# Optimization experiments

Hardware: AMD Instinct MI355X
Metric: run time of the kernel (lower is better)

## Reference

```python
import jax, jax.numpy as jnp
import numpy as np
import math

N_EMBD = 1024
N_HEAD = 16
HEAD_SIZE = N_EMBD // N_HEAD
LAYER_IDX = 2
LAMBDA_INIT = 0.8 - 0.6 * math.exp(-0.3 * (LAYER_IDX - 1))
LN_EPS = 1e-5
B, T = 4, 1024


def setup_inputs() -> dict:
    key = jax.random.key(0)
    ks = jax.random.split(key, 11)
    s = 0.02  # weight init scale
    return {
        "x": jax.random.normal(ks[0], (B, T, N_EMBD), dtype=jnp.float32),
        "Wq1": jax.random.normal(ks[1], (N_EMBD, N_EMBD), dtype=jnp.float32) * s,
        "Wq2": jax.random.normal(ks[2], (N_EMBD, N_EMBD), dtype=jnp.float32) * s,
        "Wk1": jax.random.normal(ks[3], (N_EMBD, N_EMBD), dtype=jnp.float32) * s,
        "Wk2": jax.random.normal(ks[4], (N_EMBD, N_EMBD), dtype=jnp.float32) * s,
        "Wv": jax.random.normal(ks[5], (N_EMBD, 2 * N_EMBD), dtype=jnp.float32) * s,
        "Wc": jax.random.normal(ks[6], (2 * N_EMBD, N_EMBD), dtype=jnp.float32) * s,
        "lq1": jax.random.normal(ks[7], (N_HEAD, HEAD_SIZE), dtype=jnp.float32) * 0.1,
        "lk1": jax.random.normal(ks[8], (N_HEAD, HEAD_SIZE), dtype=jnp.float32) * 0.1,
        "lq2": jax.random.normal(ks[9], (N_HEAD, HEAD_SIZE), dtype=jnp.float32) * 0.1,
        "lk2": jax.random.normal(ks[10], (N_HEAD, HEAD_SIZE), dtype=jnp.float32) * 0.1,
    }


def reference(x, Wq1, Wq2, Wk1, Wk2, Wv, Wc, lq1, lk1, lq2, lk2):
    Bx, Tx, C = x.shape
    H, hs = N_HEAD, HEAD_SIZE
    scale = 1.0 / math.sqrt(hs)

    # projections -> (B, T, H, d)
    q1 = (x @ Wq1).reshape(Bx, Tx, H, hs)
    q2 = (x @ Wq2).reshape(Bx, Tx, H, hs)
    k1 = (x @ Wk1).reshape(Bx, Tx, H, hs)
    k2 = (x @ Wk2).reshape(Bx, Tx, H, hs)
    v = (x @ Wv).reshape(Bx, Tx, H, 2 * hs)

    # dual score streams (B, H, T, T)
    att1 = jnp.einsum("bqhd,bkhd->bhqk", q1, k1) * scale
    att2 = jnp.einsum("bqhd,bkhd->bhqk", q2, k2) * scale

    causal = jnp.tril(jnp.ones((Tx, Tx), dtype=bool))  # (T, T)
    neg_inf = jnp.float32(-jnp.inf)
    att1 = jnp.where(causal, att1, neg_inf)
    att2 = jnp.where(causal, att2, neg_inf)
    a1 = jax.nn.softmax(att1, axis=-1)
    a2 = jax.nn.softmax(att2, axis=-1)

    # per-head differential lambda
    lam1 = jnp.exp(jnp.sum(lq1 * lk1, axis=-1))  # (H,)
    lam2 = jnp.exp(jnp.sum(lq2 * lk2, axis=-1))  # (H,)
    lam_full = lam1 - lam2 + LAMBDA_INIT  # (H,)

    att = a1 - lam_full[None, :, None, None] * a2  # dropout = identity (eval)

    # PV matmul -> (B, T, H, 2*hs)
    y = jnp.einsum("bhqk,bkhd->bqhd", att, v)

    # subLN over last dim (no affine)
    mu = jnp.mean(y, axis=-1, keepdims=True)
    var = jnp.mean(jnp.square(y - mu), axis=-1, keepdims=True)
    y = (y - mu) / jnp.sqrt(var + LN_EPS)
    y = y * (1.0 - LAMBDA_INIT)

    y = y.reshape(Bx, Tx, 2 * C)
    return y @ Wc  # resid dropout = identity (eval)
```

## Files before the change

kernel.cpp:

```cpp
#include <hip/hip_runtime.h>


#define T_SEQ 1024
#define NH 16
#define DV 128
#define NPROJ 6144
#define KSTR 72

typedef __bf16 bf16_t;
typedef __bf16 bf16x8 __attribute__((ext_vector_type(8)));
typedef __bf16 bf16x4 __attribute__((ext_vector_type(4)));
typedef float f32x4 __attribute__((ext_vector_type(4)));

#define LAMBDA_INIT 0.35550906759096928f
#define ONE_MINUS_LI 0.6444909324090307f
#define LOG2E 1.4426950408889634f

#define GLDS(g, l)                                                            \
  __builtin_amdgcn_global_load_lds(                                           \
      (const __attribute__((address_space(1))) void*)(g),                     \
      (__attribute__((address_space(3))) void*)(l), 16, 0, 0)

template <int C>
__device__ __forceinline__ float dppf(float x) {
  return __builtin_bit_cast(
      float, __builtin_amdgcn_update_dpp(0, __builtin_bit_cast(int, x), C,
                                         0xF, 0xF, true));
}
__device__ __forceinline__ float row16_max(float x) {
  x = fmaxf(x, dppf<0xB1>(x));
  x = fmaxf(x, dppf<0x4E>(x));
  x = fmaxf(x, dppf<0x124>(x));
  x = fmaxf(x, dppf<0x128>(x));
  return x;
}
__device__ __forceinline__ float row16_sum(float x) {
  x += dppf<0xB1>(x);
  x += dppf<0x4E>(x);
  x += dppf<0x124>(x);
  x += dppf<0x128>(x);
  return x;
}

static const size_t OFF_WCAT = 0;
static const size_t OFF_XB = OFF_WCAT + (size_t)6144 * 1024 * 2;
static const size_t OFF_WCT = OFF_XB + (size_t)4096 * 1024 * 2;
static const size_t OFF_PROJ = OFF_WCT + (size_t)2048 * 1024 * 2;
static const size_t OFF_VT = OFF_PROJ + (size_t)4096 * 6144 * 2;
static const size_t OFF_YLN = OFF_VT + (size_t)64 * 128 * 1024 * 2;
static const size_t OFF_LAM = OFF_YLN + (size_t)4096 * 2048 * 2;

__global__ void __launch_bounds__(256) cast_x(const float* __restrict__ x,
                                              bf16_t* __restrict__ o) {
  const int i = (blockIdx.x * 256 + threadIdx.x) * 4;
  float4 v = *(const float4*)(x + i);
  bf16x4 r = {(bf16_t)v.x, (bf16_t)v.y, (bf16_t)v.z, (bf16_t)v.w};
  *(bf16x4*)(o + i) = r;
}

__device__ __forceinline__ void tcast_body(const float* __restrict__ W,
                                           bf16_t* __restrict__ Wt, int K,
                                           int N, int row0) {
  __shared__ float tile[32][33];
  const int k0 = blockIdx.x * 32, n0 = blockIdx.y * 32;
  const int tx = threadIdx.x & 31, ty = threadIdx.x >> 5;
#pragma unroll
  for (int i = 0; i < 32; i += 8)
    tile[ty + i][tx] = W[(long)(k0 + ty + i) * N + n0 + tx];
  __syncthreads();
#pragma unroll
  for (int i = 0; i < 32; i += 8)
    Wt[(long)(row0 + n0 + ty + i) * K + k0 + tx] = (bf16_t)tile[tx][ty + i];
}

__global__ void __launch_bounds__(256) tcast_w(const float* __restrict__ W,
                                               bf16_t* __restrict__ Wt, int K,
                                               int N, int row0) {
  tcast_body(W, Wt, K, N, row0);
}

__global__ void __launch_bounds__(256) tcast_w4(const float* __restrict__ W0,
                                                const float* __restrict__ W1,
                                                const float* __restrict__ W2,
                                                const float* __restrict__ W3,
                                                bf16_t* __restrict__ Wt) {
  const float* Ws[4] = {W0, W1, W2, W3};
  tcast_body(Ws[blockIdx.z], Wt, 1024, 1024, blockIdx.z * 1024);
}

__global__ void lam_kernel(const float* __restrict__ lq1,
                           const float* __restrict__ lk1,
                           const float* __restrict__ lq2,
                           const float* __restrict__ lk2,
                           float* __restrict__ lam) {
  const int h = threadIdx.x;
  if (h < NH) {
    float d1 = 0.f, d2 = 0.f;
    for (int i = 0; i < 64; ++i) {
      d1 += lq1[h * 64 + i] * lk1[h * 64 + i];
      d2 += lq2[h * 64 + i] * lk2[h * 64 + i];
    }
    lam[h] = expf(d1) - expf(d2) + LAMBDA_INIT;
  }
}

#define BM 128
#define BN 128
#define BK 32

template <typename OutT>
__global__ void __launch_bounds__(256) gemm_bt(const bf16_t* __restrict__ A,
                                               const bf16_t* __restrict__ Bt,
                                               OutT* __restrict__ C, int M,
                                               int N, int K) {
  __shared__ __align__(16) bf16_t As[BM * BK];
  __shared__ __align__(16) bf16_t Bs[BN * BK];
  const int tid = threadIdx.x;
  const int w = tid >> 6;
  const int lane = tid & 63;
  const int quad = lane >> 4, l16 = lane & 15;
  const int m0 = blockIdx.y * BM, n0 = blockIdx.x * BN;
  const int wm = (w >> 1) * 64, wn = (w & 1) * 64;
  const int srow = tid >> 2;
  const int scol = (tid & 3) * 8;

  const bf16_t* Ag0 = A + (long)(m0 + srow) * K + scol;
  const bf16_t* Ag1 = Ag0 + (long)64 * K;
  const bf16_t* Bg0 = Bt + (long)(n0 + srow) * K + scol;
  const bf16_t* Bg1 = Bg0 + (long)64 * K;
  bf16_t* lA0 = As + tid * 8;
  bf16_t* lA1 = As + 2048 + tid * 8;
  bf16_t* lB0 = Bs + tid * 8;
  bf16_t* lB1 = Bs + 2048 + tid * 8;

  f32x4 acc[4][4] = {};

  for (int k0 = 0; k0 < K; k0 += BK) {
    GLDS(Ag0 + k0, lA0);
    GLDS(Ag1 + k0, lA1);
    GLDS(Bg0 + k0, lB0);
    GLDS(Bg1 + k0, lB1);
    __syncthreads();
    bf16x8 af[4], bfr[4];
#pragma unroll
    for (int t = 0; t < 4; ++t) {
      af[t] = *(const bf16x8*)(As + (wm + t * 16 + l16) * BK + quad * 8);
      bfr[t] = *(const bf16x8*)(Bs + (wn + t * 16 + l16) * BK + quad * 8);
    }
#pragma unroll
    for (int mt = 0; mt < 4; ++mt)
#pragma unroll
      for (int nt = 0; nt < 4; ++nt)
        acc[mt][nt] = __builtin_amdgcn_mfma_f32_16x16x32_bf16(
            af[mt], bfr[nt], acc[mt][nt], 0, 0, 0);
    __syncthreads();
  }

#pragma unroll
  for (int mt = 0; mt < 4; ++mt)
#pragma unroll
    for (int nt = 0; nt < 4; ++nt) {
      const int col = n0 + wn + nt * 16 + l16;
#pragma unroll
      for (int i = 0; i < 4; ++i) {
        const int row = m0 + wm + mt * 16 + quad * 4 + i;
        C[(long)row * N + col] = (OutT)acc[mt][nt][i];
      }
    }
}

__global__ void __launch_bounds__(256) transpose_v(const bf16_t* __restrict__ proj,
                                                   bf16_t* __restrict__ vt) {
  __shared__ bf16_t tile[32][34];
  const int bh = blockIdx.z;
  const int b = bh >> 4, h = bh & 15;
  const int t0 = blockIdx.x * 32, d0 = blockIdx.y * 32;
  const int tx = threadIdx.x & 31, ty = threadIdx.x >> 5;
  const bf16_t* src = proj + (long)(b * T_SEQ) * NPROJ + 4096 + h * 128;
#pragma unroll
  for (int i = 0; i < 32; i += 8)
    tile[ty + i][tx] = src[(long)(t0 + ty + i) * NPROJ + d0 + tx];
  __syncthreads();
  bf16_t* dst = vt + ((long)(b * NH + h) * DV) * T_SEQ;
#pragma unroll
  for (int i = 0; i < 32; i += 8)
    dst[(long)(d0 + ty + i) * T_SEQ + t0 + tx] = tile[tx][ty + i];
}

__global__ void __launch_bounds__(256) attn_kernel(const bf16_t* __restrict__ proj,
                                                   const bf16_t* __restrict__ vt,
                                                   const float* __restrict__ lamp,
                                                   bf16_t* __restrict__ yln) {
  const int p = blockIdx.x;
  const int h = blockIdx.y;
  const int b = blockIdx.z;
  const int tid = threadIdx.x;
  const int w = tid >> 6, lane = tid & 63;
  const int quad = lane >> 4, l16 = lane & 15;
  const long bT = (long)b * T_SEQ;

  __shared__ __align__(16) bf16_t Ks1[32 * KSTR];
  __shared__ __align__(16) bf16_t Ks2[32 * KSTR];
  __shared__ __align__(16) bf16_t Vs[DV * 32];
  __shared__ __align__(16) bf16_t pbuf[4][2][16 * 40];

  const bf16_t* gK1 =
      proj + (bT + (tid >> 3)) * (long)NPROJ + h * 64 + 2048 + (tid & 7) * 8;
  const bf16_t* gK2 = gK1 + 1024;
  const bf16_t* vbase = vt + ((long)(b * NH + h) * DV) * T_SEQ;
  const bf16_t* gV0 = vbase + (long)(tid >> 2) * T_SEQ + (tid & 3) * 8;
  const bf16_t* gV1 = gV0 + (long)64 * T_SEQ;
  const int kw = (tid >> 3) * KSTR + (tid & 7) * 8;

  bf16_t* pb1 = &pbuf[w][0][0];
  bf16_t* pb2 = &pbuf[w][1][0];
  const float sc = 0.125f * LOG2E;
  const float lam = lamp[h];
  const int prd = l16 * 40 + ((quad ^ (l16 >> 2)) << 3);

  for (int phase = 0; phase < 2; ++phase) {
    const int qblk = phase == 0 ? (15 - p) : p;
    const int q0 = qblk * 64 + w * 16;

    const bf16_t* qrow = proj + (bT + q0 + l16) * (long)NPROJ + h * 64;
    bf16x8 aq1[2], aq2[2];
    aq1[0] = *(const bf16x8*)(qrow + quad * 8);
    aq1[1] = *(const bf16x8*)(qrow + 32 + quad * 8);
    aq2[0] = *(const bf16x8*)(qrow + 1024 + quad * 8);
    aq2[1] = *(const bf16x8*)(qrow + 1024 + 32 + quad * 8);

    f32x4 O1[8] = {}, O2[8] = {};
    float m1[4], l1[4], m2[4], l2[4];
#pragma unroll
    for (int i = 0; i < 4; ++i) {
      m1[i] = -3.0e38f;
      m2[i] = -3.0e38f;
      l1[i] = 0.f;
      l2[i] = 0.f;
    }

    const int kend_blk = qblk * 64 + 64;
    const int kend_w = q0 + 16;

    bf16x8 rK1 = *(const bf16x8*)(gK1);
    bf16x8 rK2 = *(const bf16x8*)(gK2);
    bf16x8 rV0 = *(const bf16x8*)(gV0);
    bf16x8 rV1 = *(const bf16x8*)(gV1);

    for (int kt = 0; kt < kend_blk; kt += 32) {
      *(bf16x8*)(Ks1 + kw) = rK1;
      *(bf16x8*)(Ks2 + kw) = rK2;
      *(bf16x8*)(Vs + tid * 8) = rV0;
      *(bf16x8*)(Vs + 2048 + tid * 8) = rV1;
      __syncthreads();

      if (kt + 32 < kend_blk) {
        const long ko = (long)(kt + 32) * NPROJ;
        rK1 = *(const bf16x8*)(gK1 + ko);
        rK2 = *(const bf16x8*)(gK2 + ko);
        rV0 = *(const bf16x8*)(gV0 + kt + 32);
        rV1 = *(const bf16x8*)(gV1 + kt + 32);
      }

      if (kt < kend_w) {
        f32x4 s1[2], s2[2];
#pragma unroll
        for (int c = 0; c < 2; ++c) {
          const bf16_t* kr1 = Ks1 + (c * 16 + l16) * KSTR;
          const bf16_t* kr2 = Ks2 + (c * 16 + l16) * KSTR;
          bf16x8 b10 = *(const bf16x8*)(kr1 + quad * 8);
          bf16x8 b11 = *(const bf16x8*)(kr1 + 32 + quad * 8);
          f32x4 z = {};
          z = __builtin_amdgcn_mfma_f32_16x16x32_bf16(aq1[0], b10, z, 0, 0, 0);
          z = __builtin_amdgcn_mfma_f32_16x16x32_bf16(aq1[1], b11, z, 0, 0, 0);
          s1[c] = z;
          bf16x8 b20 = *(const bf16x8*)(kr2 + quad * 8);
          bf16x8 b21 = *(const bf16x8*)(kr2 + 32 + quad * 8);
          f32x4 z2 = {};
          z2 = __builtin_amdgcn_mfma_f32_16x16x32_bf16(aq2[0], b20, z2, 0, 0, 0);
          z2 = __builtin_amdgcn_mfma_f32_16x16x32_bf16(aq2[1], b21, z2, 0, 0, 0);
          s2[c] = z2;
        }
        const bool need_mask = (kt + 31 > q0);
        float t1[2][4], t2[2][4], mx1[4], mx2[4];
#pragma unroll
        for (int i = 0; i < 4; ++i) {
          mx1[i] = -3.0e38f;
          mx2[i] = -3.0e38f;
        }
#pragma unroll
        for (int c = 0; c < 2; ++c) {
          const int col = kt + c * 16 + l16;
#pragma unroll
          for (int i = 0; i < 4; ++i) {
            const int row = q0 + quad * 4 + i;
            float v1 = s1[c][i] * sc, v2 = s2[c][i] * sc;
            if (need_mask && col > row) {
              v1 = -1e30f;
              v2 = -1e30f;
            }
            t1[c][i] = v1;
            t2[c][i] = v2;
            mx1[i] = fmaxf(mx1[i], v1);
            mx2[i] = fmaxf(mx2[i], v2);
          }
        }
#pragma unroll
        for (int i = 0; i < 4; ++i) {
          mx1[i] = row16_max(mx1[i]);
          mx2[i] = row16_max(mx2[i]);
        }
        float al1[4], al2[4];
#pragma unroll
        for (int i = 0; i < 4; ++i) {
          float mn = fmaxf(m1[i], mx1[i]);
          al1[i] = exp2f(m1[i] - mn);
          m1[i] = mn;
          mn = fmaxf(m2[i], mx2[i]);
          al2[i] = exp2f(m2[i] - mn);
          m2[i] = mn;
        }
        float sum1[4] = {0, 0, 0, 0}, sum2[4] = {0, 0, 0, 0};
#pragma unroll
        for (int c = 0; c < 2; ++c) {
          const int grp0 = c * 2 + (l16 >> 3);
#pragma unroll
          for (int i = 0; i < 4; ++i) {
            bf16_t p1 = (bf16_t)exp2f(t1[c][i] - m1[i]);
            bf16_t p2 = (bf16_t)exp2f(t2[c][i] - m2[i]);
            const int off =
                (quad * 4 + i) * 40 + ((grp0 ^ quad) << 3) + (l16 & 7);
            pb1[off] = p1;
            pb2[off] = p2;
            sum1[i] += (float)p1;
            sum2[i] += (float)p2;
          }
        }
#pragma unroll
        for (int i = 0; i < 4; ++i) {
          sum1[i] = row16_sum(sum1[i]);
          sum2[i] = row16_sum(sum2[i]);
        }
#pragma unroll
        for (int i = 0; i < 4; ++i) {
          l1[i] = l1[i] * al1[i] + sum1[i];
          l2[i] = l2[i] * al2[i] + sum2[i];
        }
#pragma unroll
        for (int f = 0; f < 8; ++f)
#pragma unroll
          for (int i = 0; i < 4; ++i) {
            O1[f][i] *= al1[i];
            O2[f][i] *= al2[i];
          }
        __asm__ volatile("s_waitcnt lgkmcnt(0)" ::: "memory");
        bf16x8 ap1 = *(const bf16x8*)(pb1 + prd);
        bf16x8 ap2 = *(const bf16x8*)(pb2 + prd);
#pragma unroll
        for (int f = 0; f < 8; ++f) {
          bf16x8 bv = *(const bf16x8*)(Vs + (f * 16 + l16) * 32 + quad * 8);
          O1[f] =
              __builtin_amdgcn_mfma_f32_16x16x32_bf16(ap1, bv, O1[f], 0, 0, 0);
          O2[f] =
              __builtin_amdgcn_mfma_f32_16x16x32_bf16(ap2, bv, O2[f], 0, 0, 0);
        }
      }
      __syncthreads();
    }

    float inv1[4], inv2[4];
#pragma unroll
    for (int i = 0; i < 4; ++i) {
      inv1[i] = 1.0f / l1[i];
      inv2[i] = lam / l2[i];
    }
    float sm[4], sq[4];
#pragma unroll
    for (int i = 0; i < 4; ++i) {
      sm[i] = 0.f;
      sq[i] = 0.f;
    }
#pragma unroll
    for (int f = 0; f < 8; ++f)
#pragma unroll
      for (int i = 0; i < 4; ++i) {
        float y = O1[f][i] * inv1[i] - O2[f][i] * inv2[i];
        O1[f][i] = y;
        sm[i] += y;
        sq[i] += y * y;
      }
#pragma unroll
    for (int i = 0; i < 4; ++i) {
      sm[i] = row16_sum(sm[i]);
      sq[i] = row16_sum(sq[i]);
    }
    float mu[4], rs[4];
#pragma unroll
    for (int i = 0; i < 4; ++i) {
      mu[i] = sm[i] * (1.0f / 128.0f);
      float var = sq[i] * (1.0f / 128.0f) - mu[i] * mu[i];
      rs[i] = rsqrtf(var + 1e-5f) * ONE_MINUS_LI;
    }
#pragma unroll
    for (int i = 0; i < 4; ++i) {
      bf16_t* dst = yln + (bT + q0 + quad * 4 + i) * (long)2048 + h * 128 + l16;
#pragma unroll
      for (int f = 0; f < 8; ++f)
        dst[f * 16] = (bf16_t)((O1[f][i] - mu[i]) * rs[i]);
    }
  }
}

extern "C" void kernel_launch(void* const* d_in, const int* in_sizes, int n_in,
                              void* d_out, int out_size, void* d_ws,
                              size_t ws_size, hipStream_t stream) {
  const float* x = (const float*)d_in[0];
  const float* Wq1 = (const float*)d_in[1];
  const float* Wq2 = (const float*)d_in[2];
  const float* Wk1 = (const float*)d_in[3];
  const float* Wk2 = (const float*)d_in[4];
  const float* Wv = (const float*)d_in[5];
  const float* Wc = (const float*)d_in[6];
  const float* lq1 = (const float*)d_in[7];
  const float* lk1 = (const float*)d_in[8];
  const float* lq2 = (const float*)d_in[9];
  const float* lk2 = (const float*)d_in[10];
  float* out = (float*)d_out;

  char* ws = (char*)d_ws;
  bf16_t* wcat = (bf16_t*)(ws + OFF_WCAT);
  bf16_t* xb = (bf16_t*)(ws + OFF_XB);
  bf16_t* wct = (bf16_t*)(ws + OFF_WCT);
  bf16_t* projb = (bf16_t*)(ws + OFF_PROJ);
  bf16_t* vtb = (bf16_t*)(ws + OFF_VT);
  bf16_t* ylnb = (bf16_t*)(ws + OFF_YLN);
  float* lamp = (float*)(ws + OFF_LAM);

  cast_x<<<4096, 256, 0, stream>>>(x, xb);
  tcast_w4<<<dim3(32, 32, 4), 256, 0, stream>>>(Wq1, Wq2, Wk1, Wk2, wcat);
  tcast_w<<<dim3(32, 64), 256, 0, stream>>>(Wv, wcat, 1024, 2048, 4096);
  tcast_w<<<dim3(64, 32), 256, 0, stream>>>(Wc, wct, 2048, 1024, 0);
  lam_kernel<<<1, 64, 0, stream>>>(lq1, lk1, lq2, lk2, lamp);

  gemm_bt<bf16_t><<<dim3(48, 32), 256, 0, stream>>>(xb, wcat, projb, 4096, 6144, 1024);
  transpose_v<<<dim3(32, 4, 64), 256, 0, stream>>>(projb, vtb);
  attn_kernel<<<dim3(8, 16, 4), 256, 0, stream>>>(projb, vtb, lamp, ylnb);
  gemm_bt<float><<<dim3(8, 32), 256, 0, stream>>>(ylnb, wct, out, 4096, 1024, 2048);
}
```

Before: 368.3 us.

## Widen attention key tile to 64 and reorder grid to head-major

The attention kernel now processes 64 keys per iteration instead of 32, staging twice as much K and V in shared memory per step. Each wave issues two chained PV MFMAs per output fragment, and the V and P buffers are padded with the KSTR stride. The goal is to halve the loop trip count and the block-wide barriers, and to amortize softmax rescaling over more keys. The grid is flattened so that the head index varies fastest with the pair index. The costs are more shared memory and registers, which may lower occupancy, and more wasted masked work on diagonal tiles.

```diff
diff --git a/kernel.cpp b/kernel.cpp
--- a/kernel.cpp
+++ b/kernel.cpp
@@ -191,32 +191,32 @@
                                                    const bf16_t* __restrict__ vt,
                                                    const float* __restrict__ lamp,
                                                    bf16_t* __restrict__ yln) {
-  const int p = blockIdx.x;
-  const int h = blockIdx.y;
-  const int b = blockIdx.z;
+  const int p = blockIdx.x >> 4;
+  const int h = blockIdx.x & 15;
+  const int b = blockIdx.y;
   const int tid = threadIdx.x;
   const int w = tid >> 6, lane = tid & 63;
   const int quad = lane >> 4, l16 = lane & 15;
   const long bT = (long)b * T_SEQ;
 
-  __shared__ __align__(16) bf16_t Ks1[32 * KSTR];
-  __shared__ __align__(16) bf16_t Ks2[32 * KSTR];
-  __shared__ __align__(16) bf16_t Vs[DV * 32];
-  __shared__ __align__(16) bf16_t pbuf[4][2][16 * 40];
+  __shared__ __align__(16) bf16_t Ks1[64 * KSTR];
+  __shared__ __align__(16) bf16_t Ks2[64 * KSTR];
+  __shared__ __align__(16) bf16_t Vs[DV * KSTR];
+  __shared__ __align__(16) bf16_t pbuf[4][2][16 * KSTR];
 
   const bf16_t* gK1 =
       proj + (bT + (tid >> 3)) * (long)NPROJ + h * 64 + 2048 + (tid & 7) * 8;
   const bf16_t* gK2 = gK1 + 1024;
   const bf16_t* vbase = vt + ((long)(b * NH + h) * DV) * T_SEQ;
-  const bf16_t* gV0 = vbase + (long)(tid >> 2) * T_SEQ + (tid & 3) * 8;
-  const bf16_t* gV1 = gV0 + (long)64 * T_SEQ;
-  const int kw = (tid >> 3) * KSTR + (tid & 7) * 8;
+  const bf16_t* gV = vbase + (long)(tid >> 3) * T_SEQ + (tid & 7) * 8;
+  const int kw0 = (tid >> 3) * KSTR + (tid & 7) * 8;
 
   bf16_t* pb1 = &pbuf[w][0][0];
   bf16_t* pb2 = &pbuf[w][1][0];
   const float sc = 0.125f * LOG2E;
   const float lam = lamp[h];
-  const int prd = l16 * 40 + ((quad ^ (l16 >> 2)) << 3);
+  const int prd0 = l16 * KSTR + (((quad) ^ (l16 >> 2)) << 3);
+  const int prd1 = l16 * KSTR + (((4 + quad) ^ (l16 >> 2)) << 3);
 
   for (int phase = 0; phase < 2; ++phase) {
     const int qblk = phase == 0 ? (15 - p) : p;
@@ -242,30 +242,40 @@
     const int kend_blk = qblk * 64 + 64;
     const int kend_w = q0 + 16;
 
-    bf16x8 rK1 = *(const bf16x8*)(gK1);
-    bf16x8 rK2 = *(const bf16x8*)(gK2);
-    bf16x8 rV0 = *(const bf16x8*)(gV0);
-    bf16x8 rV1 = *(const bf16x8*)(gV1);
-
-    for (int kt = 0; kt < kend_blk; kt += 32) {
-      *(bf16x8*)(Ks1 + kw) = rK1;
-      *(bf16x8*)(Ks2 + kw) = rK2;
-      *(bf16x8*)(Vs + tid * 8) = rV0;
-      *(bf16x8*)(Vs + 2048 + tid * 8) = rV1;
+    bf16x8 rK1[2], rK2[2], rV[4];
+    rK1[0] = *(const bf16x8*)(gK1);
+    rK1[1] = *(const bf16x8*)(gK1 + (long)32 * NPROJ);
+    rK2[0] = *(const bf16x8*)(gK2);
+    rK2[1] = *(const bf16x8*)(gK2 + (long)32 * NPROJ);
+#pragma unroll
+    for (int j = 0; j < 4; ++j)
+      rV[j] = *(const bf16x8*)(gV + (long)(32 * j) * T_SEQ);
+
+    for (int kt = 0; kt < kend_blk; kt += 64) {
+      *(bf16x8*)(Ks1 + kw0) = rK1[0];
+      *(bf16x8*)(Ks1 + kw0 + 32 * KSTR) = rK1[1];
+      *(bf16x8*)(Ks2 + kw0) = rK2[0];
+      *(bf16x8*)(Ks2 + kw0 + 32 * KSTR) = rK2[1];
+#pragma unroll
+      for (int j = 0; j < 4; ++j)
+        *(bf16x8*)(Vs + kw0 + j * 32 * KSTR) = rV[j];
       __syncthreads();
 
-      if (kt + 32 < kend_blk) {
-        const long ko = (long)(kt + 32) * NPROJ;
-        rK1 = *(const bf16x8*)(gK1 + ko);
-        rK2 = *(const bf16x8*)(gK2 + ko);
-        rV0 = *(const bf16x8*)(gV0 + kt + 32);
-        rV1 = *(const bf16x8*)(gV1 + kt + 32);
+      if (kt + 64 < kend_blk) {
+        const long ko = (long)(kt + 64) * NPROJ;
+        rK1[0] = *(const bf16x8*)(gK1 + ko);
+        rK1[1] = *(const bf16x8*)(gK1 + ko + (long)32 * NPROJ);
+        rK2[0] = *(const bf16x8*)(gK2 + ko);
+        rK2[1] = *(const bf16x8*)(gK2 + ko + (long)32 * NPROJ);
+#pragma unroll
+        for (int j = 0; j < 4; ++j)
+          rV[j] = *(const bf16x8*)(gV + kt + 64 + (long)(32 * j) * T_SEQ);
       }
 
       if (kt < kend_w) {
-        f32x4 s1[2], s2[2];
-#pragma unroll
-        for (int c = 0; c < 2; ++c) {
+        f32x4 s1[4], s2[4];
+#pragma unroll
+        for (int c = 0; c < 4; ++c) {
           const bf16_t* kr1 = Ks1 + (c * 16 + l16) * KSTR;
           const bf16_t* kr2 = Ks2 + (c * 16 + l16) * KSTR;
           bf16x8 b10 = *(const bf16x8*)(kr1 + quad * 8);
@@ -281,15 +291,15 @@
           z2 = __builtin_amdgcn_mfma_f32_16x16x32_bf16(aq2[1], b21, z2, 0, 0, 0);
           s2[c] = z2;
         }
-        const bool need_mask = (kt + 31 > q0);
-        float t1[2][4], t2[2][4], mx1[4], mx2[4];
+        const bool need_mask = (kt + 63 > q0);
+        float mx1[4], mx2[4];
 #pragma unroll
         for (int i = 0; i < 4; ++i) {
           mx1[i] = -3.0e38f;
           mx2[i] = -3.0e38f;
         }
 #pragma unroll
-        for (int c = 0; c < 2; ++c) {
+        for (int c = 0; c < 4; ++c) {
           const int col = kt + c * 16 + l16;
 #pragma unroll
           for (int i = 0; i < 4; ++i) {
@@ -299,8 +309,8 @@
               v1 = -1e30f;
               v2 = -1e30f;
             }
-            t1[c][i] = v1;
-            t2[c][i] = v2;
+            s1[c][i] = v1;
+            s2[c][i] = v2;
             mx1[i] = fmaxf(mx1[i], v1);
             mx2[i] = fmaxf(mx2[i], v2);
           }
@@ -322,14 +332,14 @@
         }
         float sum1[4] = {0, 0, 0, 0}, sum2[4] = {0, 0, 0, 0};
 #pragma unroll
-        for (int c = 0; c < 2; ++c) {
-          const int grp0 = c * 2 + (l16 >> 3);
+        for (int c = 0; c < 4; ++c) {
+          const int lg = c * 2 + (l16 >> 3);
 #pragma unroll
           for (int i = 0; i < 4; ++i) {
-            bf16_t p1 = (bf16_t)exp2f(t1[c][i] - m1[i]);
-            bf16_t p2 = (bf16_t)exp2f(t2[c][i] - m2[i]);
+            bf16_t p1 = (bf16_t)exp2f(s1[c][i] - m1[i]);
+            bf16_t p2 = (bf16_t)exp2f(s2[c][i] - m2[i]);
             const int off =
-                (quad * 4 + i) * 40 + ((grp0 ^ quad) << 3) + (l16 & 7);
+                (quad * 4 + i) * KSTR + ((lg ^ quad) << 3) + (l16 & 7);
             pb1[off] = p1;
             pb2[off] = p2;
             sum1[i] += (float)p1;
@@ -354,15 +364,24 @@
             O2[f][i] *= al2[i];
           }
         __asm__ volatile("s_waitcnt lgkmcnt(0)" ::: "memory");
-        bf16x8 ap1 = *(const bf16x8*)(pb1 + prd);
-        bf16x8 ap2 = *(const bf16x8*)(pb2 + prd);
+        bf16x8 ap1[2], ap2[2];
+        ap1[0] = *(const bf16x8*)(pb1 + prd0);
+        ap1[1] = *(const bf16x8*)(pb1 + prd1);
+        ap2[0] = *(const bf16x8*)(pb2 + prd0);
+        ap2[1] = *(const bf16x8*)(pb2 + prd1);
 #pragma unroll
         for (int f = 0; f < 8; ++f) {
-          bf16x8 bv = *(const bf16x8*)(Vs + (f * 16 + l16) * 32 + quad * 8);
+          const bf16_t* vr = Vs + (f * 16 + l16) * KSTR;
+          bf16x8 bv0 = *(const bf16x8*)(vr + quad * 8);
+          bf16x8 bv1 = *(const bf16x8*)(vr + 32 + quad * 8);
           O1[f] =
-              __builtin_amdgcn_mfma_f32_16x16x32_bf16(ap1, bv, O1[f], 0, 0, 0);
+              __builtin_amdgcn_mfma_f32_16x16x32_bf16(ap1[0], bv0, O1[f], 0, 0, 0);
+          O1[f] =
+              __builtin_amdgcn_mfma_f32_16x16x32_bf16(ap1[1], bv1, O1[f], 0, 0, 0);
           O2[f] =
-              __builtin_amdgcn_mfma_f32_16x16x32_bf16(ap2, bv, O2[f], 0, 0, 0);
+              __builtin_amdgcn_mfma_f32_16x16x32_bf16(ap2[0], bv0, O2[f], 0, 0, 0);
+          O2[f] =
+              __builtin_amdgcn_mfma_f32_16x16x32_bf16(ap2[1], bv1, O2[f], 0, 0, 0);
         }
       }
       __syncthreads();
@@ -444,6 +463,6 @@
 
   gemm_bt<bf16_t><<<dim3(48, 32), 256, 0, stream>>>(xb, wcat, projb, 4096, 6144, 1024);
   transpose_v<<<dim3(32, 4, 64), 256, 0, stream>>>(projb, vtb);
-  attn_kernel<<<dim3(8, 16, 4), 256, 0, stream>>>(projb, vtb, lamp, ylnb);
+  attn_kernel<<<dim3(128, 4), 256, 0, stream>>>(projb, vtb, lamp, ylnb);
   gemm_bt<float><<<dim3(8, 32), 256, 0, stream>>>(ylnb, wct, out, 4096, 1024, 2048);
 }
```

Result: faster. 340.0 us (-7.7%).
